# Performance work log

Hardware: AMD Instinct MI355X
Metric: run time of the kernel (lower is better)

## Reference

```python
import jax, jax.numpy as jnp
import numpy as np

B, S, DIN, DOUT = 4, 2048, 4096, 4096
QMAX = 7  # int4 symmetric: values in [-8, 7]

def setup_inputs() -> dict:
    key = jax.random.key(0)
    kx, kq, ks, kb = jax.random.split(key, 4)
    x = jax.random.normal(kx, (B, S, DIN), dtype=jnp.float32)
    # int4 codes stored as int32, symmetric per-output-channel quantization
    qweight = jax.random.randint(kq, (DOUT, DIN), -8, 8, dtype=jnp.int32)
    # per-output-channel scale (max_abs / 7 style), strictly positive
    scale = jax.random.uniform(ks, (DOUT,), dtype=jnp.float32, minval=0.005, maxval=0.02)
    bias = jax.random.normal(kb, (DOUT,), dtype=jnp.float32)
    return {"x": x, "qweight": qweight, "scale": scale, "bias": bias}

def reference(x, qweight, scale, bias):
    # dequantize: per-output-channel scale broadcast over in_features
    weight = qweight.astype(jnp.float32) * scale[:, None]  # [DOUT, DIN]
    # F.linear: x @ weight.T + bias
    return jnp.einsum('bsi,oi->bso', x, weight) + bias
```

## Files before the change

kernel.cpp:

```cpp
#include <hip/hip_runtime.h>

typedef unsigned short u16;
typedef unsigned int u32;
typedef unsigned char u8;

typedef int i32x4 __attribute__((ext_vector_type(4)));

#define AS1 __attribute__((address_space(1)))
#define AS3 __attribute__((address_space(3)))

__global__ __launch_bounds__(256) void quant_x_kernel(
    const float* __restrict__ x, u8* __restrict__ xq, float* __restrict__ sx, int K)
{
    const int r = blockIdx.x;
    const int t = threadIdx.x;
    const float* xr = x + (size_t)r * K;
    float4 v[4];
    float m = 0.f;
#pragma unroll
    for (int i = 0; i < 4; ++i) {
        v[i] = *(const float4*)(xr + t * 16 + i * 4);
        m = fmaxf(m, fmaxf(fmaxf(fabsf(v[i].x), fabsf(v[i].y)),
                           fmaxf(fabsf(v[i].z), fabsf(v[i].w))));
    }
#pragma unroll
    for (int s = 32; s; s >>= 1) m = fmaxf(m, __shfl_xor(m, s));
    __shared__ float wm[4];
    if ((t & 63) == 0) wm[t >> 6] = m;
    __syncthreads();
    m = fmaxf(fmaxf(wm[0], wm[1]), fmaxf(wm[2], wm[3]));
    const float inv = 127.f / fmaxf(m, 1e-20f);
    if (t == 0) sx[r] = m * (1.f / 127.f);
    u32 o[4];
#pragma unroll
    for (int i = 0; i < 4; ++i) {
        int q0 = (int)rintf(v[i].x * inv), q1 = (int)rintf(v[i].y * inv);
        int q2 = (int)rintf(v[i].z * inv), q3 = (int)rintf(v[i].w * inv);
        o[i] = (u32)(q0 & 255) | ((u32)(q1 & 255) << 8) |
               ((u32)(q2 & 255) << 16) | ((u32)(q3 & 255) << 24);
    }
    *(uint4*)(xq + (size_t)r * K + t * 16) = make_uint4(o[0], o[1], o[2], o[3]);
}

__device__ __forceinline__ u32 pk8(int4 a) {
    return (u32)(a.x & 255) | ((u32)(a.y & 255) << 8) |
           ((u32)(a.z & 255) << 16) | ((u32)(a.w & 255) << 24);
}

__global__ void quant_w_kernel(const int4* __restrict__ q, uint4* __restrict__ y, int n16) {
    int stride = gridDim.x * blockDim.x;
    for (int i = blockIdx.x * blockDim.x + threadIdx.x; i < n16; i += stride) {
        int4 a = q[4 * i], b = q[4 * i + 1], c = q[4 * i + 2], d = q[4 * i + 3];
        y[i] = make_uint4(pk8(a), pk8(b), pk8(c), pk8(d));
    }
}


#define BM 128
#define BN 128
#define BKB 128

__global__ __launch_bounds__(256, 2) void gemm128_i8(
    const u8* __restrict__ A,
    const u8* __restrict__ W,
    const float* __restrict__ sx,
    const float* __restrict__ scale,
    const float* __restrict__ bias,
    float* __restrict__ C,
    int M, int N, int K)
{
    __shared__ alignas(1024) char lds[65536];

    const int nwg = gridDim.x;
    int bid = blockIdx.x;
    if ((nwg & 7) == 0) { int cpx = nwg >> 3; bid = (bid & 7) * cpx + (bid >> 3); }
    const int ntn = N / BN;
    const int tm = bid / ntn, tn = bid % ntn;

    const int t = threadIdx.x;
    const int l = t & 63;
    const int w = t >> 6;
    const int wm = w >> 1, wn = w & 1;
    const size_t Kz = (size_t)K;

    const int sRow = t >> 3;
    const int sCol = (((t & 7) ^ ((t >> 3) & 7)) * 16);
    const u8* aSrc = A + (size_t)(tm * BM + sRow) * Kz + sCol;
    const u8* bSrc = W + (size_t)(tn * BN + sRow) * Kz + sCol;
    const int wByte = w * 1024;

    const int rowA = (wm * 64 + (l & 15)) * 128;
    const int rowB = (wn * 64 + (l & 15)) * 128;
    const int sl0 = (((l >> 4) | 0) ^ (l & 7)) * 16;
    const int sl1 = (((l >> 4) | 4) ^ (l & 7)) * 16;

    i32x4 acc[4][4];
#pragma unroll
    for (int i = 0; i < 4; ++i)
#pragma unroll
        for (int j = 0; j < 4; ++j) acc[i][j] = (i32x4){0, 0, 0, 0};

    const int NT = K / BKB;

    auto stageTile = [&](int b, int kt) {
        char* dA = lds + b * 32768 + wByte;
        char* dB = lds + b * 32768 + 16384 + wByte;
#pragma unroll
        for (int c = 0; c < 4; ++c)
            __builtin_amdgcn_global_load_lds(
                (const AS1 void*)(aSrc + (size_t)c * 32 * Kz + (size_t)kt * BKB),
                (AS3 void*)(dA + c * 4096), 16, 0, 0);
#pragma unroll
        for (int c = 0; c < 4; ++c)
            __builtin_amdgcn_global_load_lds(
                (const AS1 void*)(bSrc + (size_t)c * 32 * Kz + (size_t)kt * BKB),
                (AS3 void*)(dB + c * 4096), 16, 0, 0);
    };

    stageTile(0, 0);
    asm volatile("s_waitcnt vmcnt(0)" ::: "memory");
    __builtin_amdgcn_s_barrier();

#pragma unroll 1
    for (int p = 0; p < NT; ++p) {
        const int cur = p & 1;
        stageTile(cur ^ 1, (p + 1) & (NT - 1));

        const char* aB = lds + cur * 32768 + rowA;
        const char* bB = lds + cur * 32768 + 16384 + rowB;
        i32x4 aF[2][4], bF[2][4];
#pragma unroll
        for (int f = 0; f < 4; ++f) aF[0][f] = *(const i32x4*)(aB + f * 2048 + sl0);
#pragma unroll
        for (int f = 0; f < 4; ++f) bF[0][f] = *(const i32x4*)(bB + f * 2048 + sl0);
#pragma unroll
        for (int f = 0; f < 4; ++f) aF[1][f] = *(const i32x4*)(aB + f * 2048 + sl1);
#pragma unroll
        for (int f = 0; f < 4; ++f) bF[1][f] = *(const i32x4*)(bB + f * 2048 + sl1);

        __builtin_amdgcn_s_setprio(1);
#pragma unroll
        for (int ks = 0; ks < 2; ++ks)
#pragma unroll
            for (int f = 0; f < 4; ++f)
#pragma unroll
                for (int fn = 0; fn < 4; ++fn)
                    acc[f][fn] = __builtin_amdgcn_mfma_i32_16x16x64_i8(
                        bF[ks][fn], aF[ks][f], acc[f][fn], 0, 0, 0);
        __builtin_amdgcn_s_setprio(0);

        asm volatile("s_waitcnt vmcnt(0) lgkmcnt(0)" ::: "memory");
        __builtin_amdgcn_s_barrier();
    }

    const int mB = tm * BM + wm * 64 + (l & 15);
    const int nB = tn * BN + wn * 64 + 4 * (l >> 4);
    float sxv[4];
#pragma unroll
    for (int f = 0; f < 4; ++f) sxv[f] = sx[mB + f * 16];
#pragma unroll
    for (int fn = 0; fn < 4; ++fn) {
        const int n0 = nB + fn * 16;
        const float4 s4 = *(const float4*)(scale + n0);
        const float4 b4 = *(const float4*)(bias + n0);
#pragma unroll
        for (int f = 0; f < 4; ++f) {
            const int m = mB + f * 16;
            const float sm = sxv[f];
            float4 v;
            v.x = (float)acc[f][fn][0] * (sm * s4.x) + b4.x;
            v.y = (float)acc[f][fn][1] * (sm * s4.y) + b4.y;
            v.z = (float)acc[f][fn][2] * (sm * s4.z) + b4.z;
            v.w = (float)acc[f][fn][3] * (sm * s4.w) + b4.w;
            *(float4*)(C + (size_t)m * N + n0) = v;
        }
    }
}

extern "C" void kernel_launch(void* const* d_in, const int* in_sizes, int n_in,
                              void* d_out, int out_size, void* d_ws, size_t ws_size,
                              hipStream_t stream) {
    const float* x     = (const float*)d_in[0];
    const int*   qw    = (const int*)d_in[1];
    const float* scale = (const float*)d_in[2];
    const float* bias  = (const float*)d_in[3];
    float*       out   = (float*)d_out;

    const int N = in_sizes[2];
    const int K = in_sizes[1] / N;
    const int M = in_sizes[0] / K;

    u8*    xq = (u8*)d_ws;
    u8*    wq = xq + (size_t)M * K;
    float* sx = (float*)(wq + (size_t)N * K);

    quant_x_kernel<<<M, 256, 0, stream>>>(x, xq, sx, K);
    quant_w_kernel<<<2048, 256, 0, stream>>>((const int4*)qw, (uint4*)wq, (N * K) / 16);

    const int grid = (M / BM) * (N / BN);
    gemm128_i8<<<grid, 256, 0, stream>>>(xq, wq, sx, scale, bias, out, M, N, K);
}
```

Baseline: 200.3 us.

## Enlarge int8 GEMM tile to 256x256 and fuse quantization kernels

The GEMM block tile grows from 128x128 to 256x256. Each wave now computes a 128x128 sub-tile with an 8x8 grid of MFMA accumulators, which inline asm pins to AGPRs, and the double-buffered LDS doubles to 128KB. The aim is to halve global and LDS traffic per MFMA and raise arithmetic intensity. In exchange, occupancy drops to one block per CU and the grid shrinks to 512 tiles. The x and weight quantization kernels are also merged into one launch to save a kernel launch and let both pieces run concurrently.

```diff
diff --git a/kernel.cpp b/kernel.cpp
--- a/kernel.cpp
+++ b/kernel.cpp
@@ -1,6 +1,5 @@
 #include <hip/hip_runtime.h>
 
-typedef unsigned short u16;
 typedef unsigned int u32;
 typedef unsigned char u8;
 
@@ -8,59 +7,62 @@
 
 #define AS1 __attribute__((address_space(1)))
 #define AS3 __attribute__((address_space(3)))
-
-__global__ __launch_bounds__(256) void quant_x_kernel(
-    const float* __restrict__ x, u8* __restrict__ xq, float* __restrict__ sx, int K)
-{
-    const int r = blockIdx.x;
-    const int t = threadIdx.x;
-    const float* xr = x + (size_t)r * K;
-    float4 v[4];
-    float m = 0.f;
-#pragma unroll
-    for (int i = 0; i < 4; ++i) {
-        v[i] = *(const float4*)(xr + t * 16 + i * 4);
-        m = fmaxf(m, fmaxf(fmaxf(fabsf(v[i].x), fabsf(v[i].y)),
-                           fmaxf(fabsf(v[i].z), fabsf(v[i].w))));
-    }
-#pragma unroll
-    for (int s = 32; s; s >>= 1) m = fmaxf(m, __shfl_xor(m, s));
-    __shared__ float wm[4];
-    if ((t & 63) == 0) wm[t >> 6] = m;
-    __syncthreads();
-    m = fmaxf(fmaxf(wm[0], wm[1]), fmaxf(wm[2], wm[3]));
-    const float inv = 127.f / fmaxf(m, 1e-20f);
-    if (t == 0) sx[r] = m * (1.f / 127.f);
-    u32 o[4];
-#pragma unroll
-    for (int i = 0; i < 4; ++i) {
-        int q0 = (int)rintf(v[i].x * inv), q1 = (int)rintf(v[i].y * inv);
-        int q2 = (int)rintf(v[i].z * inv), q3 = (int)rintf(v[i].w * inv);
-        o[i] = (u32)(q0 & 255) | ((u32)(q1 & 255) << 8) |
-               ((u32)(q2 & 255) << 16) | ((u32)(q3 & 255) << 24);
-    }
-    *(uint4*)(xq + (size_t)r * K + t * 16) = make_uint4(o[0], o[1], o[2], o[3]);
-}
 
 __device__ __forceinline__ u32 pk8(int4 a) {
     return (u32)(a.x & 255) | ((u32)(a.y & 255) << 8) |
            ((u32)(a.z & 255) << 16) | ((u32)(a.w & 255) << 24);
 }
 
-__global__ void quant_w_kernel(const int4* __restrict__ q, uint4* __restrict__ y, int n16) {
-    int stride = gridDim.x * blockDim.x;
-    for (int i = blockIdx.x * blockDim.x + threadIdx.x; i < n16; i += stride) {
-        int4 a = q[4 * i], b = q[4 * i + 1], c = q[4 * i + 2], d = q[4 * i + 3];
-        y[i] = make_uint4(pk8(a), pk8(b), pk8(c), pk8(d));
+__global__ __launch_bounds__(256) void quant_xw_kernel(
+    const float* __restrict__ x, u8* __restrict__ xq, float* __restrict__ sx,
+    const int4* __restrict__ qw, uint4* __restrict__ wq,
+    int K, int M, int n16)
+{
+    const int b = blockIdx.x;
+    const int t = threadIdx.x;
+    if (b < M) {
+        const float* xr = x + (size_t)b * K;
+        float4 v[4];
+        float m = 0.f;
+#pragma unroll
+        for (int i = 0; i < 4; ++i) {
+            v[i] = *(const float4*)(xr + t * 16 + i * 4);
+            m = fmaxf(m, fmaxf(fmaxf(fabsf(v[i].x), fabsf(v[i].y)),
+                               fmaxf(fabsf(v[i].z), fabsf(v[i].w))));
+        }
+#pragma unroll
+        for (int s = 32; s; s >>= 1) m = fmaxf(m, __shfl_xor(m, s));
+        __shared__ float wm[4];
+        if ((t & 63) == 0) wm[t >> 6] = m;
+        __syncthreads();
+        m = fmaxf(fmaxf(wm[0], wm[1]), fmaxf(wm[2], wm[3]));
+        const float inv = 127.f / fmaxf(m, 1e-20f);
+        if (t == 0) sx[b] = m * (1.f / 127.f);
+        u32 o[4];
+#pragma unroll
+        for (int i = 0; i < 4; ++i) {
+            int q0 = (int)rintf(v[i].x * inv), q1 = (int)rintf(v[i].y * inv);
+            int q2 = (int)rintf(v[i].z * inv), q3 = (int)rintf(v[i].w * inv);
+            o[i] = (u32)(q0 & 255) | ((u32)(q1 & 255) << 8) |
+                   ((u32)(q2 & 255) << 16) | ((u32)(q3 & 255) << 24);
+        }
+        *(uint4*)(xq + (size_t)b * K + t * 16) = make_uint4(o[0], o[1], o[2], o[3]);
+    } else {
+        const int nb = gridDim.x - M;
+        const int stride = nb * 256;
+        for (int i = (b - M) * 256 + t; i < n16; i += stride) {
+            int4 a = qw[4 * i], c = qw[4 * i + 1], d = qw[4 * i + 2], e = qw[4 * i + 3];
+            wq[i] = make_uint4(pk8(a), pk8(c), pk8(d), pk8(e));
+        }
     }
 }
 
 
-#define BM 128
-#define BN 128
+#define BM 256
+#define BN 256
 #define BKB 128
 
-__global__ __launch_bounds__(256, 2) void gemm128_i8(
+__global__ __launch_bounds__(256, 1) void gemm256_i8a(
     const u8* __restrict__ A,
     const u8* __restrict__ W,
     const float* __restrict__ sx,
@@ -69,7 +71,7 @@
     float* __restrict__ C,
     int M, int N, int K)
 {
-    __shared__ alignas(1024) char lds[65536];
+    __shared__ alignas(1024) char lds[131072];
 
     const int nwg = gridDim.x;
     int bid = blockIdx.x;
@@ -89,29 +91,29 @@
     const u8* bSrc = W + (size_t)(tn * BN + sRow) * Kz + sCol;
     const int wByte = w * 1024;
 
-    const int rowA = (wm * 64 + (l & 15)) * 128;
-    const int rowB = (wn * 64 + (l & 15)) * 128;
+    const int rowA = (wm * 128 + (l & 15)) * 128;
+    const int rowB = (wn * 128 + (l & 15)) * 128;
     const int sl0 = (((l >> 4) | 0) ^ (l & 7)) * 16;
     const int sl1 = (((l >> 4) | 4) ^ (l & 7)) * 16;
 
-    i32x4 acc[4][4];
-#pragma unroll
-    for (int i = 0; i < 4; ++i)
-#pragma unroll
-        for (int j = 0; j < 4; ++j) acc[i][j] = (i32x4){0, 0, 0, 0};
+    i32x4 acc[8][8];
+#pragma unroll
+    for (int i = 0; i < 8; ++i)
+#pragma unroll
+        for (int j = 0; j < 8; ++j) acc[i][j] = (i32x4){0, 0, 0, 0};
 
     const int NT = K / BKB;
 
     auto stageTile = [&](int b, int kt) {
-        char* dA = lds + b * 32768 + wByte;
-        char* dB = lds + b * 32768 + 16384 + wByte;
-#pragma unroll
-        for (int c = 0; c < 4; ++c)
+        char* dA = lds + b * 65536 + wByte;
+        char* dB = lds + b * 65536 + 32768 + wByte;
+#pragma unroll
+        for (int c = 0; c < 8; ++c)
             __builtin_amdgcn_global_load_lds(
                 (const AS1 void*)(aSrc + (size_t)c * 32 * Kz + (size_t)kt * BKB),
                 (AS3 void*)(dA + c * 4096), 16, 0, 0);
 #pragma unroll
-        for (int c = 0; c < 4; ++c)
+        for (int c = 0; c < 8; ++c)
             __builtin_amdgcn_global_load_lds(
                 (const AS1 void*)(bSrc + (size_t)c * 32 * Kz + (size_t)kt * BKB),
                 (AS3 void*)(dB + c * 4096), 16, 0, 0);
@@ -126,45 +128,44 @@
         const int cur = p & 1;
         stageTile(cur ^ 1, (p + 1) & (NT - 1));
 
-        const char* aB = lds + cur * 32768 + rowA;
-        const char* bB = lds + cur * 32768 + 16384 + rowB;
-        i32x4 aF[2][4], bF[2][4];
-#pragma unroll
-        for (int f = 0; f < 4; ++f) aF[0][f] = *(const i32x4*)(aB + f * 2048 + sl0);
-#pragma unroll
-        for (int f = 0; f < 4; ++f) bF[0][f] = *(const i32x4*)(bB + f * 2048 + sl0);
-#pragma unroll
-        for (int f = 0; f < 4; ++f) aF[1][f] = *(const i32x4*)(aB + f * 2048 + sl1);
-#pragma unroll
-        for (int f = 0; f < 4; ++f) bF[1][f] = *(const i32x4*)(bB + f * 2048 + sl1);
-
-        __builtin_amdgcn_s_setprio(1);
-#pragma unroll
-        for (int ks = 0; ks < 2; ++ks)
-#pragma unroll
-            for (int f = 0; f < 4; ++f)
-#pragma unroll
-                for (int fn = 0; fn < 4; ++fn)
-                    acc[f][fn] = __builtin_amdgcn_mfma_i32_16x16x64_i8(
-                        bF[ks][fn], aF[ks][f], acc[f][fn], 0, 0, 0);
-        __builtin_amdgcn_s_setprio(0);
+        const char* aB = lds + cur * 65536 + rowA;
+        const char* bB = lds + cur * 65536 + 32768 + rowB;
+
+#pragma unroll
+        for (int ks = 0; ks < 2; ++ks) {
+            const int sl = ks ? sl1 : sl0;
+            i32x4 aF[8], bF[8];
+#pragma unroll
+            for (int f = 0; f < 8; ++f) aF[f] = *(const i32x4*)(aB + f * 2048 + sl);
+#pragma unroll
+            for (int f = 0; f < 8; ++f) bF[f] = *(const i32x4*)(bB + f * 2048 + sl);
+            __builtin_amdgcn_s_setprio(1);
+#pragma unroll
+            for (int f = 0; f < 8; ++f)
+#pragma unroll
+                for (int fn = 0; fn < 8; ++fn)
+                    asm("v_mfma_i32_16x16x64_i8 %0, %1, %2, %0"
+                        : "+a"(acc[f][fn])
+                        : "v"(bF[fn]), "v"(aF[f]));
+            __builtin_amdgcn_s_setprio(0);
+        }
 
         asm volatile("s_waitcnt vmcnt(0) lgkmcnt(0)" ::: "memory");
         __builtin_amdgcn_s_barrier();
     }
 
-    const int mB = tm * BM + wm * 64 + (l & 15);
-    const int nB = tn * BN + wn * 64 + 4 * (l >> 4);
-    float sxv[4];
-#pragma unroll
-    for (int f = 0; f < 4; ++f) sxv[f] = sx[mB + f * 16];
-#pragma unroll
-    for (int fn = 0; fn < 4; ++fn) {
+    const int mB = tm * BM + wm * 128 + (l & 15);
+    const int nB = tn * BN + wn * 128 + 4 * (l >> 4);
+    float sxv[8];
+#pragma unroll
+    for (int f = 0; f < 8; ++f) sxv[f] = sx[mB + f * 16];
+#pragma unroll
+    for (int fn = 0; fn < 8; ++fn) {
         const int n0 = nB + fn * 16;
         const float4 s4 = *(const float4*)(scale + n0);
         const float4 b4 = *(const float4*)(bias + n0);
 #pragma unroll
-        for (int f = 0; f < 4; ++f) {
+        for (int f = 0; f < 8; ++f) {
             const int m = mB + f * 16;
             const float sm = sxv[f];
             float4 v;
@@ -194,9 +195,10 @@
     u8*    wq = xq + (size_t)M * K;
     float* sx = (float*)(wq + (size_t)N * K);
 
-    quant_x_kernel<<<M, 256, 0, stream>>>(x, xq, sx, K);
-    quant_w_kernel<<<2048, 256, 0, stream>>>((const int4*)qw, (uint4*)wq, (N * K) / 16);
+    const int n16 = (N * K) / 16;
+    quant_xw_kernel<<<M + 512, 256, 0, stream>>>(x, xq, sx, (const int4*)qw,
+                                                 (uint4*)wq, K, M, n16);
 
     const int grid = (M / BM) * (N / BN);
-    gemm128_i8<<<grid, 256, 0, stream>>>(xq, wq, sx, scale, bias, out, M, N, K);
-}
+    gemm256_i8a<<<grid, 256, 0, stream>>>(xq, wq, sx, scale, bias, out, M, N, K);
+}
```

Measured after the change: 196.0 us. -2.1%, faster.
